# Performance work log

Measured on AMD Instinct MI355X. Metric: run time of the kernel, lower is better.

## Reference

```python
import jax, jax.numpy as jnp
import numpy as np

N_LEADS = 12

def _norm_adj():
    """Normalized adjacency matching GCNConv semantics on the fixed ECG graph.
    The buffer adj already includes eye(12); PyG GCNConv (add_self_loops=True)
    adds one more self-loop of weight 1, so effective self-weight is 2.
    A_norm = D^{-1/2} A_eff D^{-1/2}.
    """
    adj = np.zeros((N_LEADS, N_LEADS), dtype=np.float32)
    conns = [(0, 1), (0, 2), (1, 2), (0, 3), (1, 3), (2, 3), (0, 4), (1, 4), (1, 5), (2, 5),
             (6, 7), (7, 8), (8, 9), (9, 10), (10, 11)]
    for i, j in conns:
        adj[i, j] = 1.0
        adj[j, i] = 1.0
    a_eff = adj + 2.0 * np.eye(N_LEADS, dtype=np.float32)  # buffer eye + PyG self-loop
    deg = a_eff.sum(axis=1)
    dinv = 1.0 / np.sqrt(deg)
    return jnp.asarray(dinv[:, None] * a_eff * dinv[None, :])

A_NORM = _norm_adj()  # (12, 12)

def setup_inputs() -> dict:
    key = jax.random.key(0)
    ks = jax.random.split(key, 7)
    B, F_IN, H, OUT = 16384, 512, 256, 128
    s = 0.02
    return {
        "x": jax.random.normal(ks[0], (B, N_LEADS, F_IN), dtype=jnp.float32),
        "W1": jax.random.normal(ks[1], (F_IN, H), dtype=jnp.float32) * s,
        "b1": jnp.zeros((H,), dtype=jnp.float32),
        "W2": jax.random.normal(ks[2], (H, H), dtype=jnp.float32) * s,
        "b2": jnp.zeros((H,), dtype=jnp.float32),
        "W3": jax.random.normal(ks[3], (H, OUT), dtype=jnp.float32) * s,
        "b3": jnp.zeros((OUT,), dtype=jnp.float32),
    }

def _gcn(a, x, w, b):
    # GCNConv: A_norm @ (X W) + b, batched over b. Shapes: x (B,12,f), w (f,o)
    return jnp.einsum("nm,bmo->bno", a, jnp.einsum("bnf,fo->bno", x, w)) + b

def reference(x, W1, b1, W2, b2, W3, b3):
    a = A_NORM.astype(x.dtype)
    h = jax.nn.relu(_gcn(a, x, W1, b1))   # dropout is identity in eval mode
    h = jax.nn.relu(_gcn(a, h, W2, b2))
    h = _gcn(a, h, W3, b3)                # (B, 12, out)
    x_mean = h.mean(axis=1)
    x_max = h.max(axis=1)
    return jnp.concatenate([x_mean, x_max], axis=1)  # (B, 2*out)
```

## Files before the change

kernel.cpp:

```cpp
#include <hip/hip_runtime.h>
#include <math.h>

typedef _Float16 f16x8 __attribute__((ext_vector_type(8)));
typedef _Float16 f16x2 __attribute__((ext_vector_type(2)));
typedef float    f32x4 __attribute__((ext_vector_type(4)));

namespace {
constexpr unsigned kMask[12] = {0x01Eu,0x03Du,0x02Bu,0x007u,0x003u,0x006u,
                                0x080u,0x140u,0x280u,0x500u,0xA00u,0x400u};
constexpr int kDeg[12] = {6,7,6,5,4,4,3,4,4,4,4,3};
}

template<int K, int N, bool IN_F16, bool RELU, bool POOL>
__global__ __launch_bounds__(512)
void gcn_layer(const void* __restrict__ inp,
               const _Float16* __restrict__ wt,
               const float* __restrict__ bias,
               void* __restrict__ outp)
{
    constexpr int NT  = N / 64;
    constexpr int AST = 72;
    constexpr int ABYTES = 96 * AST * 2;
    constexpr int WBYTES = N * AST * 2;
    constexpr int STAGE_BYTES = ABYTES + WBYTES;
    constexpr int POOL_BYTES  = 96 * 129 * 4;
    constexpr int SMEM = (POOL && POOL_BYTES > STAGE_BYTES) ? POOL_BYTES : STAGE_BYTES;

    __shared__ __align__(16) char smem[SMEM];
    _Float16* Abuf = (_Float16*)smem;
    _Float16* Wbuf = (_Float16*)(smem + ABYTES);

    const int tid  = threadIdx.x;
    const int lane = tid & 63;
    const int wave = tid >> 6;
    const int wm   = wave & 1;
    const int wn   = wave >> 1;
    const int l15  = lane & 15;
    const int q    = lane >> 4;

    const long rowbase = (long)blockIdx.x * 96;

    float dinv[12];
    #pragma unroll
    for (int r = 0; r < 12; ++r) dinv[r] = 1.0f / sqrtf((float)kDeg[r]);

    f32x4 acc[3][NT];
    #pragma unroll
    for (int a = 0; a < 3; ++a)
        #pragma unroll
        for (int b = 0; b < NT; ++b)
            acc[a][b] = (f32x4){0.f, 0.f, 0.f, 0.f};

    for (int kc = 0; kc < K / 64; ++kc) {
        if (tid < 256) {
            const int g  = tid >> 5;
            const int f2 = tid & 31;
            float2 y[12];
            #pragma unroll
            for (int n = 0; n < 12; ++n) {
                const long off = (rowbase + g*12 + n) * K + kc*64 + f2*2;
                float vx, vy;
                if (IN_F16) {
                    const _Float16* p = (const _Float16*)inp + off;
                    vx = (float)p[0]; vy = (float)p[1];
                } else {
                    const float* p = (const float*)inp + off;
                    vx = p[0]; vy = p[1];
                }
                y[n].x = dinv[n] * vx;
                y[n].y = dinv[n] * vy;
            }
            #pragma unroll
            for (int r = 0; r < 12; ++r) {
                float sx = 2.0f * y[r].x;
                float sy = 2.0f * y[r].y;
                #pragma unroll
                for (int j = 0; j < 12; ++j) {
                    if ((kMask[r] >> j) & 1u) { sx += y[j].x; sy += y[j].y; }
                }
                sx *= dinv[r]; sy *= dinv[r];
                f16x2 h2; h2.x = (_Float16)sx; h2.y = (_Float16)sy;
                *(f16x2*)&Abuf[(g*12 + r) * AST + f2*2] = h2;
            }
        } else {
            const int t2   = tid - 256;
            const int k8   = t2 & 7;
            const int orow = t2 >> 3;
            #pragma unroll
            for (int pass = 0; pass < N / 32; ++pass) {
                const int o = pass*32 + orow;
                const uint4 d = *(const uint4*)(wt + (long)o*K + kc*64 + k8*8);
                *(uint4*)&Wbuf[o*AST + k8*8] = d;
            }
        }
        __syncthreads();

        #pragma unroll
        for (int ks = 0; ks < 2; ++ks) {
            f16x8 af[3];
            f16x8 bf[NT];
            #pragma unroll
            for (int tm = 0; tm < 3; ++tm)
                af[tm] = *(const f16x8*)&Abuf[(wm*48 + tm*16 + l15)*AST + ks*32 + q*8];
            #pragma unroll
            for (int tn = 0; tn < NT; ++tn)
                bf[tn] = *(const f16x8*)&Wbuf[(wn*NT*16 + tn*16 + l15)*AST + ks*32 + q*8];
            #pragma unroll
            for (int tm = 0; tm < 3; ++tm)
                #pragma unroll
                for (int tn = 0; tn < NT; ++tn)
                    acc[tm][tn] = __builtin_amdgcn_mfma_f32_16x16x32_f16(
                        af[tm], bf[tn], acc[tm][tn], 0, 0, 0);
        }
        __syncthreads();
    }

    if (!POOL) {
        _Float16* hout = (_Float16*)outp;
        float bcol[NT];
        #pragma unroll
        for (int tn = 0; tn < NT; ++tn) bcol[tn] = bias[wn*NT*16 + tn*16 + l15];
        #pragma unroll
        for (int tm = 0; tm < 3; ++tm) {
            #pragma unroll
            for (int tn = 0; tn < NT; ++tn) {
                #pragma unroll
                for (int r = 0; r < 4; ++r) {
                    const long row = rowbase + wm*48 + tm*16 + q*4 + r;
                    const int  col = wn*NT*16 + tn*16 + l15;
                    float v = acc[tm][tn][r] + bcol[tn];
                    if (RELU) v = fmaxf(v, 0.0f);
                    hout[row*N + col] = (_Float16)v;
                }
            }
        }
    } else {
        float* C = (float*)smem;
        #pragma unroll
        for (int tm = 0; tm < 3; ++tm)
            #pragma unroll
            for (int tn = 0; tn < NT; ++tn)
                #pragma unroll
                for (int r = 0; r < 4; ++r) {
                    const int row = wm*48 + tm*16 + q*4 + r;
                    const int col = wn*NT*16 + tn*16 + l15;
                    C[row*129 + col] = acc[tm][tn][r];
                }
        __syncthreads();
        float* out = (float*)outp;
        #pragma unroll
        for (int p = 0; p < 2; ++p) {
            const int idx = tid + p*512;
            const int bl  = idx >> 7;
            const int col = idx & 127;
            float s = 0.0f, mx = -INFINITY;
            #pragma unroll
            for (int n = 0; n < 12; ++n) {
                const float v = C[(bl*12 + n)*129 + col];
                s += v; mx = fmaxf(mx, v);
            }
            const float b  = bias[col];
            const long  ob = ((long)blockIdx.x*8 + bl) * 256;
            out[ob + col]       = s / 12.0f + b;
            out[ob + 128 + col] = mx + b;
        }
    }
}

__global__ void prep_weights(const float* __restrict__ W1,
                             const float* __restrict__ W2,
                             const float* __restrict__ W3,
                             _Float16* __restrict__ wt)
{
    const int tid = blockIdx.x * 256 + threadIdx.x;
    constexpr int N1 = 512*256, N2 = 256*256, N3 = 256*128;
    if (tid < N1) {
        const int o = tid >> 9, k = tid & 511;
        wt[tid] = (_Float16)W1[k*256 + o];
    } else if (tid < N1 + N2) {
        const int t = tid - N1;
        const int o = t >> 8, k = t & 255;
        wt[N1 + t] = (_Float16)W2[k*256 + o];
    } else if (tid < N1 + N2 + N3) {
        const int t = tid - N1 - N2;
        const int o = t >> 8, k = t & 255;
        wt[N1 + N2 + t] = (_Float16)W3[k*128 + o];
    }
}

extern "C" void kernel_launch(void* const* d_in, const int* in_sizes, int n_in,
                              void* d_out, int out_size, void* d_ws, size_t ws_size,
                              hipStream_t stream)
{
    const float* x  = (const float*)d_in[0];
    const float* W1 = (const float*)d_in[1];
    const float* b1 = (const float*)d_in[2];
    const float* W2 = (const float*)d_in[3];
    const float* b2 = (const float*)d_in[4];
    const float* W3 = (const float*)d_in[5];
    const float* b3 = (const float*)d_in[6];
    float* out = (float*)d_out;

    _Float16* wt  = (_Float16*)d_ws;
    _Float16* wt1 = wt;
    _Float16* wt2 = wt + 512*256;
    _Float16* wt3 = wt + 512*256 + 256*256;
    _Float16* h1  = wt + 512*256 + 256*256 + 256*128;
    _Float16* h2  = h1 + (long)196608 * 256;

    prep_weights<<<896, 256, 0, stream>>>(W1, W2, W3, wt);

    gcn_layer<512, 256, false, true,  false><<<2048, 512, 0, stream>>>(x,  wt1, b1, h1);
    gcn_layer<256, 256, true,  true,  false><<<2048, 512, 0, stream>>>(h1, wt2, b2, h2);
    gcn_layer<256, 128, true,  false, true ><<<2048, 512, 0, stream>>>(h2, wt3, b3, out);
}
```

Baseline: 652.6 us.

## Fuse three GCN layers into one kernel with LDS-resident hidden activations

Replaces the three per-layer launches with a single kernel. Each 96-row block keeps its hidden activations in LDS between layers, so the fp16 h1/h2 round-trips through global memory go away. It also adds register prefetching of the next K-chunk of x and weights, with a barrier that waits only on LDS counters, so global loads can overlap the MFMA work. LDS per block grows with the extra hidden buffer, which may reduce occupancy.

```diff
diff --git a/kernel.cpp b/kernel.cpp
--- a/kernel.cpp
+++ b/kernel.cpp
@@ -9,161 +9,220 @@
 constexpr unsigned kMask[12] = {0x01Eu,0x03Du,0x02Bu,0x007u,0x003u,0x006u,
                                 0x080u,0x140u,0x280u,0x500u,0xA00u,0x400u};
 constexpr int kDeg[12] = {6,7,6,5,4,4,3,4,4,4,4,3};
-}
-
-template<int K, int N, bool IN_F16, bool RELU, bool POOL>
+
+constexpr int AST = 72;
+constexpr int HST = 260;
+constexpr int ABYTES = 96  * AST * 2;
+constexpr int WBYTES = 256 * AST * 2;
+constexpr int HBYTES = 96  * HST * 2;
+constexpr int SMEM   = ABYTES + WBYTES + HBYTES;
+}
+
+__device__ __forceinline__ void barrier_keep_vmcnt()
+{
+    __builtin_amdgcn_sched_barrier(0);
+    asm volatile("s_waitcnt lgkmcnt(0)" ::: "memory");
+    __builtin_amdgcn_s_barrier();
+    __builtin_amdgcn_sched_barrier(0);
+}
+
+template<int K, int N, bool SRC_LDS>
+__device__ __forceinline__ void run_layer(
+    const float*    __restrict__ xg,
+    const _Float16* __restrict__ hs,
+    const _Float16* __restrict__ wt,
+    _Float16* __restrict__ Abuf,
+    _Float16* __restrict__ Wbuf,
+    long rowbase, int tid,
+    f32x4 (&acc)[3][N/64])
+{
+    constexpr int NT = N / 64, KC = K / 64, NPASS = N / 32;
+    const int lane = tid & 63, wave = tid >> 6;
+    const int wm = wave & 1, wn = wave >> 1;
+    const int l15 = lane & 15, q = lane >> 4;
+
+    float dinv[12];
+    #pragma unroll
+    for (int r = 0; r < 12; ++r) dinv[r] = 1.0f / sqrtf((float)kDeg[r]);
+
+    #pragma unroll
+    for (int a = 0; a < 3; ++a)
+        #pragma unroll
+        for (int b = 0; b < NT; ++b)
+            acc[a][b] = (f32x4){0.f, 0.f, 0.f, 0.f};
+
+    const int g  = tid >> 5, f2 = tid & 31;
+    const int t2 = tid - 256, k8 = t2 & 7, orow = t2 >> 3;
+
+    float2 y[12];
+    uint4  wreg[NPASS];
+
+    if (tid < 256) {
+        if constexpr (!SRC_LDS) {
+            #pragma unroll
+            for (int n = 0; n < 12; ++n) {
+                const float* p = xg + (rowbase + g*12 + n) * (long)K + f2*2;
+                y[n].x = p[0]; y[n].y = p[1];
+            }
+        }
+    } else {
+        #pragma unroll
+        for (int pass = 0; pass < NPASS; ++pass)
+            wreg[pass] = *(const uint4*)(wt + (long)(pass*32 + orow) * K + k8*8);
+    }
+
+    for (int kc = 0; kc < KC; ++kc) {
+        if (tid < 256) {
+            if constexpr (SRC_LDS) {
+                #pragma unroll
+                for (int n = 0; n < 12; ++n) {
+                    const f16x2 h2 = *(const f16x2*)&hs[(g*12 + n)*HST + kc*64 + f2*2];
+                    y[n].x = (float)h2.x; y[n].y = (float)h2.y;
+                }
+            }
+            float2 ys[12];
+            #pragma unroll
+            for (int n = 0; n < 12; ++n) {
+                ys[n].x = dinv[n] * y[n].x;
+                ys[n].y = dinv[n] * y[n].y;
+            }
+            #pragma unroll
+            for (int r = 0; r < 12; ++r) {
+                float sx = 2.0f * ys[r].x;
+                float sy = 2.0f * ys[r].y;
+                #pragma unroll
+                for (int j = 0; j < 12; ++j)
+                    if ((kMask[r] >> j) & 1u) { sx += ys[j].x; sy += ys[j].y; }
+                sx *= dinv[r]; sy *= dinv[r];
+                f16x2 h2; h2.x = (_Float16)sx; h2.y = (_Float16)sy;
+                *(f16x2*)&Abuf[(g*12 + r)*AST + f2*2] = h2;
+            }
+            if constexpr (!SRC_LDS) {
+                if (kc + 1 < KC) {
+                    #pragma unroll
+                    for (int n = 0; n < 12; ++n) {
+                        const float* p = xg + (rowbase + g*12 + n) * (long)K
+                                            + (kc + 1)*64 + f2*2;
+                        y[n].x = p[0]; y[n].y = p[1];
+                    }
+                }
+            }
+        } else {
+            #pragma unroll
+            for (int pass = 0; pass < NPASS; ++pass)
+                *(uint4*)&Wbuf[(pass*32 + orow)*AST + k8*8] = wreg[pass];
+            if (kc + 1 < KC) {
+                #pragma unroll
+                for (int pass = 0; pass < NPASS; ++pass)
+                    wreg[pass] = *(const uint4*)(wt + (long)(pass*32 + orow) * K
+                                                    + (kc + 1)*64 + k8*8);
+            }
+        }
+        barrier_keep_vmcnt();
+
+        #pragma unroll
+        for (int ks = 0; ks < 2; ++ks) {
+            f16x8 af[3], bf[NT];
+            #pragma unroll
+            for (int tm = 0; tm < 3; ++tm)
+                af[tm] = *(const f16x8*)&Abuf[(wm*48 + tm*16 + l15)*AST + ks*32 + q*8];
+            #pragma unroll
+            for (int tn = 0; tn < NT; ++tn)
+                bf[tn] = *(const f16x8*)&Wbuf[(wn*NT*16 + tn*16 + l15)*AST + ks*32 + q*8];
+            #pragma unroll
+            for (int tm = 0; tm < 3; ++tm)
+                #pragma unroll
+                for (int tn = 0; tn < NT; ++tn)
+                    acc[tm][tn] = __builtin_amdgcn_mfma_f32_16x16x32_f16(
+                        af[tm], bf[tn], acc[tm][tn], 0, 0, 0);
+        }
+        barrier_keep_vmcnt();
+    }
+}
+
+template<int N>
+__device__ __forceinline__ void store_h(
+    f32x4 (&acc)[3][N/64], const float* __restrict__ bias,
+    _Float16* __restrict__ H, int tid)
+{
+    constexpr int NT = N / 64;
+    const int lane = tid & 63, wave = tid >> 6;
+    const int wm = wave & 1, wn = wave >> 1;
+    const int l15 = lane & 15, q = lane >> 4;
+    float bcol[NT];
+    #pragma unroll
+    for (int tn = 0; tn < NT; ++tn) bcol[tn] = bias[wn*NT*16 + tn*16 + l15];
+    #pragma unroll
+    for (int tm = 0; tm < 3; ++tm)
+        #pragma unroll
+        for (int tn = 0; tn < NT; ++tn)
+            #pragma unroll
+            for (int r = 0; r < 4; ++r) {
+                const int row = wm*48 + tm*16 + q*4 + r;
+                const int col = wn*NT*16 + tn*16 + l15;
+                H[row*HST + col] = (_Float16)fmaxf(acc[tm][tn][r] + bcol[tn], 0.f);
+            }
+}
+
 __global__ __launch_bounds__(512)
-void gcn_layer(const void* __restrict__ inp,
-               const _Float16* __restrict__ wt,
-               const float* __restrict__ bias,
-               void* __restrict__ outp)
-{
-    constexpr int NT  = N / 64;
-    constexpr int AST = 72;
-    constexpr int ABYTES = 96 * AST * 2;
-    constexpr int WBYTES = N * AST * 2;
-    constexpr int STAGE_BYTES = ABYTES + WBYTES;
-    constexpr int POOL_BYTES  = 96 * 129 * 4;
-    constexpr int SMEM = (POOL && POOL_BYTES > STAGE_BYTES) ? POOL_BYTES : STAGE_BYTES;
-
+void gcn_fused(const float* __restrict__ x,
+               const _Float16* __restrict__ wt1, const float* __restrict__ b1,
+               const _Float16* __restrict__ wt2, const float* __restrict__ b2,
+               const _Float16* __restrict__ wt3, const float* __restrict__ b3,
+               float* __restrict__ out)
+{
     __shared__ __align__(16) char smem[SMEM];
     _Float16* Abuf = (_Float16*)smem;
     _Float16* Wbuf = (_Float16*)(smem + ABYTES);
-
-    const int tid  = threadIdx.x;
-    const int lane = tid & 63;
-    const int wave = tid >> 6;
-    const int wm   = wave & 1;
-    const int wn   = wave >> 1;
-    const int l15  = lane & 15;
-    const int q    = lane >> 4;
-
+    _Float16* Hbuf = (_Float16*)(smem + ABYTES + WBYTES);
+
+    const int tid = threadIdx.x;
     const long rowbase = (long)blockIdx.x * 96;
 
-    float dinv[12];
-    #pragma unroll
-    for (int r = 0; r < 12; ++r) dinv[r] = 1.0f / sqrtf((float)kDeg[r]);
-
-    f32x4 acc[3][NT];
-    #pragma unroll
-    for (int a = 0; a < 3; ++a)
-        #pragma unroll
-        for (int b = 0; b < NT; ++b)
-            acc[a][b] = (f32x4){0.f, 0.f, 0.f, 0.f};
-
-    for (int kc = 0; kc < K / 64; ++kc) {
-        if (tid < 256) {
-            const int g  = tid >> 5;
-            const int f2 = tid & 31;
-            float2 y[12];
-            #pragma unroll
-            for (int n = 0; n < 12; ++n) {
-                const long off = (rowbase + g*12 + n) * K + kc*64 + f2*2;
-                float vx, vy;
-                if (IN_F16) {
-                    const _Float16* p = (const _Float16*)inp + off;
-                    vx = (float)p[0]; vy = (float)p[1];
-                } else {
-                    const float* p = (const float*)inp + off;
-                    vx = p[0]; vy = p[1];
-                }
-                y[n].x = dinv[n] * vx;
-                y[n].y = dinv[n] * vy;
-            }
-            #pragma unroll
-            for (int r = 0; r < 12; ++r) {
-                float sx = 2.0f * y[r].x;
-                float sy = 2.0f * y[r].y;
-                #pragma unroll
-                for (int j = 0; j < 12; ++j) {
-                    if ((kMask[r] >> j) & 1u) { sx += y[j].x; sy += y[j].y; }
-                }
-                sx *= dinv[r]; sy *= dinv[r];
-                f16x2 h2; h2.x = (_Float16)sx; h2.y = (_Float16)sy;
-                *(f16x2*)&Abuf[(g*12 + r) * AST + f2*2] = h2;
-            }
-        } else {
-            const int t2   = tid - 256;
-            const int k8   = t2 & 7;
-            const int orow = t2 >> 3;
-            #pragma unroll
-            for (int pass = 0; pass < N / 32; ++pass) {
-                const int o = pass*32 + orow;
-                const uint4 d = *(const uint4*)(wt + (long)o*K + kc*64 + k8*8);
-                *(uint4*)&Wbuf[o*AST + k8*8] = d;
-            }
-        }
-        __syncthreads();
-
-        #pragma unroll
-        for (int ks = 0; ks < 2; ++ks) {
-            f16x8 af[3];
-            f16x8 bf[NT];
-            #pragma unroll
-            for (int tm = 0; tm < 3; ++tm)
-                af[tm] = *(const f16x8*)&Abuf[(wm*48 + tm*16 + l15)*AST + ks*32 + q*8];
-            #pragma unroll
-            for (int tn = 0; tn < NT; ++tn)
-                bf[tn] = *(const f16x8*)&Wbuf[(wn*NT*16 + tn*16 + l15)*AST + ks*32 + q*8];
-            #pragma unroll
-            for (int tm = 0; tm < 3; ++tm)
-                #pragma unroll
-                for (int tn = 0; tn < NT; ++tn)
-                    acc[tm][tn] = __builtin_amdgcn_mfma_f32_16x16x32_f16(
-                        af[tm], bf[tn], acc[tm][tn], 0, 0, 0);
-        }
-        __syncthreads();
-    }
-
-    if (!POOL) {
-        _Float16* hout = (_Float16*)outp;
-        float bcol[NT];
-        #pragma unroll
-        for (int tn = 0; tn < NT; ++tn) bcol[tn] = bias[wn*NT*16 + tn*16 + l15];
-        #pragma unroll
-        for (int tm = 0; tm < 3; ++tm) {
-            #pragma unroll
-            for (int tn = 0; tn < NT; ++tn) {
-                #pragma unroll
-                for (int r = 0; r < 4; ++r) {
-                    const long row = rowbase + wm*48 + tm*16 + q*4 + r;
-                    const int  col = wn*NT*16 + tn*16 + l15;
-                    float v = acc[tm][tn][r] + bcol[tn];
-                    if (RELU) v = fmaxf(v, 0.0f);
-                    hout[row*N + col] = (_Float16)v;
-                }
-            }
-        }
-    } else {
-        float* C = (float*)smem;
+    f32x4 acc[3][4];
+    run_layer<512, 256, false>(x, nullptr, wt1, Abuf, Wbuf, rowbase, tid, acc);
+    store_h<256>(acc, b1, Hbuf, tid);
+    __syncthreads();
+
+    run_layer<256, 256, true>(nullptr, Hbuf, wt2, Abuf, Wbuf, rowbase, tid, acc);
+    store_h<256>(acc, b2, Hbuf, tid);
+    __syncthreads();
+
+    f32x4 acc3[3][2];
+    run_layer<256, 128, true>(nullptr, Hbuf, wt3, Abuf, Wbuf, rowbase, tid, acc3);
+
+    float* C = (float*)smem;
+    {
+        const int lane = tid & 63, wave = tid >> 6;
+        const int wm = wave & 1, wn = wave >> 1;
+        const int l15 = lane & 15, q = lane >> 4;
         #pragma unroll
         for (int tm = 0; tm < 3; ++tm)
             #pragma unroll
-            for (int tn = 0; tn < NT; ++tn)
+            for (int tn = 0; tn < 2; ++tn)
                 #pragma unroll
                 for (int r = 0; r < 4; ++r) {
                     const int row = wm*48 + tm*16 + q*4 + r;
-                    const int col = wn*NT*16 + tn*16 + l15;
-                    C[row*129 + col] = acc[tm][tn][r];
+                    const int col = wn*32 + tn*16 + l15;
+                    C[row*129 + col] = acc3[tm][tn][r];
                 }
-        __syncthreads();
-        float* out = (float*)outp;
-        #pragma unroll
-        for (int p = 0; p < 2; ++p) {
-            const int idx = tid + p*512;
-            const int bl  = idx >> 7;
-            const int col = idx & 127;
-            float s = 0.0f, mx = -INFINITY;
-            #pragma unroll
-            for (int n = 0; n < 12; ++n) {
-                const float v = C[(bl*12 + n)*129 + col];
-                s += v; mx = fmaxf(mx, v);
-            }
-            const float b  = bias[col];
-            const long  ob = ((long)blockIdx.x*8 + bl) * 256;
-            out[ob + col]       = s / 12.0f + b;
-            out[ob + 128 + col] = mx + b;
-        }
+    }
+    __syncthreads();
+    #pragma unroll
+    for (int p = 0; p < 2; ++p) {
+        const int idx = tid + p*512;
+        const int bl  = idx >> 7;
+        const int col = idx & 127;
+        float s = 0.0f, mx = -INFINITY;
+        #pragma unroll
+        for (int n = 0; n < 12; ++n) {
+            const float v = C[(bl*12 + n)*129 + col];
+            s += v; mx = fmaxf(mx, v);
+        }
+        const float b  = b3[col];
+        const long  ob = ((long)blockIdx.x*8 + bl) * 256;
+        out[ob + col]       = s / 12.0f + b;
+        out[ob + 128 + col] = mx + b;
     }
 }
 
@@ -205,12 +264,7 @@
     _Float16* wt1 = wt;
     _Float16* wt2 = wt + 512*256;
     _Float16* wt3 = wt + 512*256 + 256*256;
-    _Float16* h1  = wt + 512*256 + 256*256 + 256*128;
-    _Float16* h2  = h1 + (long)196608 * 256;
 
     prep_weights<<<896, 256, 0, stream>>>(W1, W2, W3, wt);
-
-    gcn_layer<512, 256, false, true,  false><<<2048, 512, 0, stream>>>(x,  wt1, b1, h1);
-    gcn_layer<256, 256, true,  true,  false><<<2048, 512, 0, stream>>>(h1, wt2, b2, h2);
-    gcn_layer<256, 128, true,  false, true ><<<2048, 512, 0, stream>>>(h2, wt3, b3, out);
-}
+    gcn_fused<<<2048, 512, 0, stream>>>(x, wt1, b1, wt2, b2, wt3, b3, out);
+}
```

New measurement: 796.0 us. +22.0%, slower.
